# Optimization experiments

Hardware: AMD Instinct MI355X
Metric: run time of the kernel (lower is better)

The kernel has to match this reference:

```python
import jax, jax.numpy as jnp
import numpy as np

L, NK = 4, 6  # num blocks, Nk geodesic components

def _gelu(x):
    return jax.nn.gelu(x, approximate=False)  # torch nn.GELU default (erf)

def _ln(x, g, b, eps=1e-5):
    m = jnp.mean(x, axis=-1, keepdims=True)
    v = jnp.mean((x - m) ** 2, axis=-1, keepdims=True)
    return (x - m) * jax.lax.rsqrt(v + eps) * g + b


def setup_inputs() -> dict:
    B, N, C, M = 4, 8192, 64, 64
    key = jax.random.key(0)
    ks = iter(jax.random.split(key, 48))
    def nrm(*s):
        return jax.random.normal(next(ks), s, dtype=jnp.float32) * 0.02
    inp = {
        'x': jax.random.normal(next(ks), (B, N, 1), dtype=jnp.float32),
        'MATRIX_Phy': jax.random.normal(next(ks), (N, M), dtype=jnp.float32) * 0.02,
        'INVERSE_Phy': jax.random.normal(next(ks), (M, N), dtype=jnp.float32) * 0.02,
        'meshPoints': jax.random.normal(next(ks), (N, 3), dtype=jnp.float32),
        'adj_norm': jax.random.uniform(next(ks), (N, N), dtype=jnp.float32) / N,
    }
    inp.update(
        fc0_w=nrm(4, C), fc0_b=jnp.zeros(C), fc01_w=nrm(C, C), fc01_b=jnp.zeros(C),
        blk_ln1_g=jnp.ones((L, C)), blk_ln1_b=jnp.zeros((L, C)),
        norm1_g=jnp.ones((L, C)), norm1_b=jnp.zeros((L, C)),
        spec_w=jax.random.uniform(next(ks), (L, NK, C, C, M), dtype=jnp.float32) / (C * C),
        enc_p1_w=nrm(L, 3, C), enc_p1_b=jnp.zeros((L, C)),
        enc_p2_w=nrm(L, C, C), enc_p2_b=jnp.zeros((L, C)),
        enc_g1_w=nrm(L, C, C), enc_g1_b=jnp.zeros((L, C)),
        enc_g2_w=nrm(L, C, C), enc_g2_b=jnp.zeros((L, C)),
        enc_o1_w=nrm(L, C, 2 * C), enc_o1_b=jnp.zeros((L, 2 * C)),
        enc_o2_w=nrm(L, 2 * C, NK), enc_o2_b=jnp.zeros((L, NK)),
        spat_g1_w=nrm(L, C, 2 * C), spat_g1_b=jnp.zeros((L, 2 * C)),
        spat_g2_w=nrm(L, 2 * C, C), spat_g2_b=jnp.zeros((L, C)),
        blk_ln2_g=jnp.ones((L, C)), blk_ln2_b=jnp.zeros((L, C)),
        mlp_pre_w=nrm(L, C, 2 * C), mlp_pre_b=jnp.zeros((L, 2 * C)),
        mlp_post_w=nrm(L, 2 * C, C), mlp_post_b=jnp.zeros((L, C)),
        ln1_g=jnp.ones(C), ln1_b=jnp.zeros(C),
        fc1_w=nrm(C, 128), fc1_b=jnp.zeros(128),
        fc2_w=nrm(128, 1), fc2_b=jnp.zeros(1),
    )
    return inp


def reference(x, MATRIX_Phy, INVERSE_Phy, meshPoints, adj_norm,
              fc0_w, fc0_b, fc01_w, fc01_b,
              blk_ln1_g, blk_ln1_b, norm1_g, norm1_b, spec_w,
              enc_p1_w, enc_p1_b, enc_p2_w, enc_p2_b,
              enc_g1_w, enc_g1_b, enc_g2_w, enc_g2_b,
              enc_o1_w, enc_o1_b, enc_o2_w, enc_o2_b,
              spat_g1_w, spat_g1_b, spat_g2_w, spat_g2_b,
              blk_ln2_g, blk_ln2_b, mlp_pre_w, mlp_pre_b, mlp_post_w, mlp_post_b,
              ln1_g, ln1_b, fc1_w, fc1_b, fc2_w, fc2_b):
    B = x.shape[0]
    mesh = jnp.broadcast_to(meshPoints[None], (B,) + meshPoints.shape)  # [B,N,3]
    h = jnp.concatenate([x, mesh], axis=-1)                             # [B,N,4]
    h = h @ fc0_w + fc0_b
    h = h @ fc01_w + fc01_b                                             # [B,N,C]
    for l in range(L):
        z = _ln(h, blk_ln1_g[l], blk_ln1_b[l])
        # --- MeshGCN encoder -> geodesic mixing coefficients geoT [M,Nk] ---
        e = _gelu(meshPoints @ enc_p1_w[l] + enc_p1_b[l]) @ enc_p2_w[l] + enc_p2_b[l]
        e = _gelu(adj_norm @ (e @ enc_g1_w[l] + enc_g1_b[l]))
        e = adj_norm @ (e @ enc_g2_w[l] + enc_g2_b[l])
        e = (e @ enc_o1_w[l] + enc_o1_b[l]) @ enc_o2_w[l] + enc_o2_b[l]  # [N,Nk]
        geoT = jax.nn.softmax(INVERSE_Phy @ e, axis=1)                   # [M,Nk]
        # --- geodesic-modulated spectral conv ---
        cm = jnp.einsum('mn,bnc->bcm', INVERSE_Phy, z)                   # [B,C,M]
        w = jnp.einsum('kiom,mk->iom', spec_w[l], geoT)                  # [C,C,M]
        cg = jnp.einsum('bim,iom->bom', cm, w)                           # [B,C,M]
        x1 = jnp.einsum('bom,nm->bno', cg, MATRIX_Phy)                   # [B,N,C]
        x1 = _ln(x1, norm1_g[l], norm1_b[l])
        # --- spatial GCN branch (SimpleGCN: gcn->relu->gcn) ---
        s = jax.nn.relu(jnp.einsum('mn,bnc->bmc', adj_norm, z @ spat_g1_w[l] + spat_g1_b[l]))
        x2 = jnp.einsum('mn,bnc->bmc', adj_norm, s @ spat_g2_w[l] + spat_g2_b[l])
        h = x1 + x2 + h
        z2 = _ln(h, blk_ln2_g[l], blk_ln2_b[l])
        h = _gelu(z2 @ mlp_pre_w[l] + mlp_pre_b[l]) @ mlp_post_w[l] + mlp_post_b[l] + h
    h = _gelu(_ln(h, ln1_g, ln1_b) @ fc1_w + fc1_b)
    return h @ fc2_w + fc2_b                                             # [B,N,1]
```

## Files before the change

kernel.cpp:

```cpp
#include <hip/hip_runtime.h>
#include <math.h>

typedef __bf16 bf16_t;
typedef __bf16 bf16x8 __attribute__((ext_vector_type(8)));
typedef __bf16 bf16x4 __attribute__((ext_vector_type(4)));
typedef float  f32x4  __attribute__((ext_vector_type(4)));
typedef float  f32x16 __attribute__((ext_vector_type(16)));

#define NN 8192
#define RA 8320
#define GPS256 2129920u
#define XPAD 68
#define X2PAD 132
#define ZTPAD 66

__device__ __forceinline__ float gelu_f(float x) {
    return 0.5f * x * (1.0f + erff(x * 0.70710678118654752f));
}

__device__ __forceinline__ float wsum64(float v) {
#pragma unroll
    for (int m = 32; m; m >>= 1) v += __shfl_xor(v, m);
    return v;
}

__device__ __forceinline__ float gpn(const float* __restrict__ Gp, size_t gi, size_t st, int ns) {
    float v = Gp[gi];
    if (ns == 2) v += Gp[gi + st];
    return v;
}

__device__ __forceinline__ void async16(const void* g, void* l) {
    __builtin_amdgcn_global_load_lds(
        (const __attribute__((address_space(1))) unsigned int*)g,
        (__attribute__((address_space(3))) unsigned int*)l,
        16, 0, 0);
}

__device__ __forceinline__ void mm16(const float* __restrict__ X, int xpad,
                                     const float* __restrict__ W, int ws, int K,
                                     int c, int r0, float* acc) {
    for (int k0 = 0; k0 < K; k0 += 4) {
        float w0 = W[(size_t)(k0 + 0) * ws + c];
        float w1 = W[(size_t)(k0 + 1) * ws + c];
        float w2 = W[(size_t)(k0 + 2) * ws + c];
        float w3 = W[(size_t)(k0 + 3) * ws + c];
#pragma unroll
        for (int i = 0; i < 16; ++i) {
            float4 xv = *(const float4*)(X + (size_t)(r0 + i) * xpad + k0);
            acc[i] = fmaf(xv.x, w0, acc[i]);
            acc[i] = fmaf(xv.y, w1, acc[i]);
            acc[i] = fmaf(xv.z, w2, acc[i]);
            acc[i] = fmaf(xv.w, w3, acc[i]);
        }
    }
}

__global__ __launch_bounds__(256) void k_adj_convert(const float* __restrict__ adj,
                                                     const float* __restrict__ INV,
                                                     bf16_t* __restrict__ adjB,
                                                     float* __restrict__ rowsum) {
    int row = blockIdx.x;
    int t = threadIdx.x;
    bf16_t* br = adjB + (size_t)row * NN;
    if (row >= NN + 64) {
        bf16x4 zz; zz[0] = zz[1] = zz[2] = zz[3] = (bf16_t)0.f;
#pragma unroll
        for (int v = 0; v < 8; ++v) *(bf16x4*)(br + (v * 256 + t) * 4) = zz;
        return;
    }
    const float* ar = (row < NN) ? adj + (size_t)row * NN : INV + (size_t)(row - NN) * NN;
    float s = 0.f;
#pragma unroll
    for (int v = 0; v < 8; ++v) {
        int i = (v * 256 + t) * 4;
        float4 f = *(const float4*)(ar + i);
        s += f.x + f.y + f.z + f.w;
        bf16x4 o;
        o[0] = (bf16_t)f.x; o[1] = (bf16_t)f.y; o[2] = (bf16_t)f.z; o[3] = (bf16_t)f.w;
        *(bf16x4*)(br + i) = o;
    }
    if (row < NN) {
        s = wsum64(s);
        __shared__ float w4[4];
        if ((t & 63) == 0) w4[t >> 6] = s;
        __syncthreads();
        if (t == 0) rowsum[row] = w4[0] + w4[1] + w4[2] + w4[3];
    }
}

__global__ __launch_bounds__(64) void k_fold(const float* __restrict__ fc0w, const float* __restrict__ fc0b,
                                             const float* __restrict__ fc01w, const float* __restrict__ fc01b,
                                             float* __restrict__ W0b) {
    int c = threadIdx.x;
#pragma unroll
    for (int j = 0; j < 4; ++j) {
        float a = 0.f;
        for (int k = 0; k < 64; ++k) a += fc0w[j * 64 + k] * fc01w[k * 64 + c];
        W0b[j * 64 + c] = a;
    }
    float b = fc01b[c];
    for (int k = 0; k < 64; ++k) b += fc0b[k] * fc01w[k * 64 + c];
    W0b[256 + c] = b;
}

__global__ __launch_bounds__(256) void k_init_h(const float* __restrict__ x, const float* __restrict__ mesh,
                         const float* __restrict__ W0b,
                         const float* __restrict__ zg, const float* __restrict__ zb,
                         float* __restrict__ h, bf16_t* __restrict__ Vt) {
    __shared__ __align__(16) char buf[64 * ZTPAD * 2];
    bf16_t* ZT = (bf16_t*)buf;
    int t = threadIdx.x, c = t & 63, rq = t >> 6, r0 = rq * 16;
    int bb = blockIdx.x >> 7, n0 = (blockIdx.x & 127) * 64;
    float w0c = W0b[c], w1c = W0b[64 + c], w2c = W0b[128 + c], w3c = W0b[192 + c], b0c = W0b[256 + c];
    float gc = zg[c], bc = zb[c];
#pragma unroll
    for (int q = 0; q < 16; ++q) {
        int n = n0 + r0 + q;
        int w = bb * NN + n;
        float xv = x[w];
        float m0 = mesh[n * 3], m1 = mesh[n * 3 + 1], m2 = mesh[n * 3 + 2];
        float hv = b0c + xv * w0c + m0 * w1c + m1 * w2c + m2 * w3c;
        h[(size_t)w * 64 + c] = hv;
        float s = wsum64(hv), s2 = wsum64(hv * hv);
        float mean = s * (1.f / 64.f), var = s2 * (1.f / 64.f) - mean * mean;
        float z = (hv - mean) * rsqrtf(var + 1e-5f) * gc + bc;
        ZT[c * ZTPAD + r0 + q] = (bf16_t)z;
    }
    __syncthreads();
#pragma unroll
    for (int cc = 0; cc < 16; ++cc) {
        int c2 = r0 + cc;
        Vt[(size_t)(256 + bb * 64 + c2) * NN + n0 + c] = ZT[c2 * ZTPAD + c];
    }
}

__global__ __launch_bounds__(256) void k_enc_pre(const float* __restrict__ mesh,
                          const float* __restrict__ p1w, const float* __restrict__ p1b,
                          const float* __restrict__ p2w, const float* __restrict__ p2b,
                          const float* __restrict__ g1w, const float* __restrict__ g1b,
                          bf16_t* __restrict__ Vt) {
    __shared__ __align__(16) char buf[2 * 64 * XPAD * 4];
    float* X1 = (float*)buf;
    float* X2 = (float*)(buf + 64 * XPAD * 4);
    bf16_t* ZT = (bf16_t*)buf;
    int t = threadIdx.x, c = t & 63, rq = t >> 6, r0 = rq * 16;
    int ll = blockIdx.x >> 7, n0 = (blockIdx.x & 127) * 64;
    float p1b_c = p1b[ll * 64 + c];
    float p1w0 = p1w[(ll * 3 + 0) * 64 + c], p1w1 = p1w[(ll * 3 + 1) * 64 + c], p1w2 = p1w[(ll * 3 + 2) * 64 + c];
#pragma unroll
    for (int q = 0; q < 16; ++q) {
        int n = n0 + r0 + q;
        float m0 = mesh[n * 3], m1 = mesh[n * 3 + 1], m2 = mesh[n * 3 + 2];
        X1[(r0 + q) * XPAD + c] = gelu_f(p1b_c + m0 * p1w0 + m1 * p1w1 + m2 * p1w2);
    }
    __syncthreads();
    float e2[16];
#pragma unroll
    for (int i = 0; i < 16; ++i) e2[i] = p2b[ll * 64 + c];
    mm16(X1, XPAD, p2w + ll * 4096, 64, 64, c, r0, e2);
    __syncthreads();
#pragma unroll
    for (int q = 0; q < 16; ++q) X2[(r0 + q) * XPAD + c] = e2[q];
    __syncthreads();
    float tt[16];
#pragma unroll
    for (int i = 0; i < 16; ++i) tt[i] = g1b[ll * 64 + c];
    mm16(X2, XPAD, g1w + ll * 4096, 64, 64, c, r0, tt);
#pragma unroll
    for (int q = 0; q < 16; ++q) ZT[c * ZTPAD + r0 + q] = (bf16_t)tt[q];
    __syncthreads();
#pragma unroll
    for (int cc = 0; cc < 16; ++cc) {
        int c2 = r0 + cc;
        Vt[(size_t)(ll * 64 + c2) * NN + n0 + c] = ZT[c2 * ZTPAD + c];
    }
}

__global__ __launch_bounds__(256) void k_enc_mid(const float* __restrict__ Gp,
                          const float* __restrict__ g2w, const float* __restrict__ g2b,
                          bf16_t* __restrict__ Vt) {
    __shared__ __align__(16) char buf[64 * XPAD * 4 + 64 * ZTPAD * 2];
    float* X = (float*)buf;
    bf16_t* ZT = (bf16_t*)(buf + 64 * XPAD * 4);
    int t = threadIdx.x, c = t & 63, rq = t >> 6, r0 = rq * 16;
    int ll = blockIdx.x >> 7, n0 = (blockIdx.x & 127) * 64;
#pragma unroll
    for (int q = 0; q < 16; ++q) {
        int n = n0 + r0 + q;
        size_t gi = (size_t)n * 256 + ll * 64 + c;
        X[(r0 + q) * XPAD + c] = gelu_f(Gp[gi] + Gp[gi + GPS256]);
    }
    __syncthreads();
    float t2[16];
#pragma unroll
    for (int i = 0; i < 16; ++i) t2[i] = g2b[ll * 64 + c];
    mm16(X, XPAD, g2w + ll * 4096, 64, 64, c, r0, t2);
#pragma unroll
    for (int q = 0; q < 16; ++q) ZT[c * ZTPAD + r0 + q] = (bf16_t)t2[q];
    __syncthreads();
#pragma unroll
    for (int cc = 0; cc < 16; ++cc) {
        int c2 = r0 + cc;
        Vt[(size_t)(ll * 64 + c2) * NN + n0 + c] = ZT[c2 * ZTPAD + c];
    }
}

__global__ void k_geo_part(const float* __restrict__ Gp,
                           const float* __restrict__ o1w, const float* __restrict__ o1b,
                           const float* __restrict__ o2w, const float* __restrict__ o2b,
                           const float* __restrict__ INV,
                           float* __restrict__ partials) {
    int l = blockIdx.x >> 7, chunk = blockIdx.x & 127;
    int n0 = chunk * 64;
    int t = threadIdx.x;
    __shared__ float e4L[64][65];
    for (int r = 0; r < 64; ++r)
        e4L[r][t] = Gp[(size_t)(n0 + r) * 512 + l * 64 + t];
    __syncthreads();
    float X[64];
#pragma unroll
    for (int i = 0; i < 64; ++i) X[i] = e4L[t][i];
    float e5[6] = {0, 0, 0, 0, 0, 0};
    const float* o1wl = o1w + (size_t)l * 64 * 128;
    const float* o2wl = o2w + (size_t)l * 128 * 6;
    for (int j = 0; j < 128; ++j) {
        float a = o1b[l * 128 + j];
#pragma unroll
        for (int i = 0; i < 64; ++i) a += X[i] * o1wl[i * 128 + j];
#pragma unroll
        for (int k = 0; k < 6; ++k) e5[k] += a * o2wl[j * 6 + k];
    }
#pragma unroll
    for (int k = 0; k < 6; ++k) e5[k] += o2b[l * 6 + k];
    __shared__ float e5L[64][8];
#pragma unroll
    for (int k = 0; k < 6; ++k) e5L[t][k] = e5[k];
    __syncthreads();
    float p[6] = {0, 0, 0, 0, 0, 0};
    const float* ivr = INV + (size_t)t * NN + n0;
    for (int r = 0; r < 64; ++r) {
        float iv = ivr[r];
#pragma unroll
        for (int k = 0; k < 6; ++k) p[k] += iv * e5L[r][k];
    }
#pragma unroll
    for (int k = 0; k < 6; ++k) partials[(size_t)(((l * 128 + chunk) * 64) + t) * 6 + k] = p[k];
}

__global__ void k_geo_final(const float* __restrict__ partials, float* __restrict__ geoT) {
    int l = blockIdx.x, m = threadIdx.x;
    float g[6] = {0, 0, 0, 0, 0, 0};
    for (int ch = 0; ch < 128; ++ch) {
#pragma unroll
        for (int k = 0; k < 6; ++k) g[k] += partials[(size_t)(((l * 128 + ch) * 64) + m) * 6 + k];
    }
    float mx = g[0];
#pragma unroll
    for (int k = 1; k < 6; ++k) mx = fmaxf(mx, g[k]);
    float s = 0.f;
#pragma unroll
    for (int k = 0; k < 6; ++k) { g[k] = expf(g[k] - mx); s += g[k]; }
    float inv = 1.f / s;
#pragma unroll
    for (int k = 0; k < 6; ++k) geoT[(size_t)(l * 64 + m) * 6 + k] = g[k] * inv;
}

__global__ __launch_bounds__(64) void k_w(const float* __restrict__ specw,
                                          const float* __restrict__ geoT,
                                          float* __restrict__ wAll) {
    int l = blockIdx.x >> 12, io = blockIdx.x & 4095;
    int m = threadIdx.x;
    float a = 0.f;
#pragma unroll
    for (int k = 0; k < 6; ++k)
        a += specw[(((size_t)l * 6 + k) * 4096 + io) * 64 + m] * geoT[(size_t)(l * 64 + m) * 6 + k];
    wAll[((size_t)l * 4096 + io) * 64 + m] = a;
}

__global__ __launch_bounds__(256) void k_cmsum(const float* __restrict__ Gp, float* __restrict__ cmc,
                                               int ncols, int colbase, int ns) {
    int bi = blockIdx.x * 4 + (threadIdx.x >> 6);
    int m = threadIdx.x & 63;
    size_t st = (size_t)RA * ncols;
    size_t gi = (size_t)(NN + m) * ncols + colbase + bi;
    cmc[bi * 64 + m] = gpn(Gp, gi, st, ns);
}

__global__ __launch_bounds__(256) void k_cg2(const float* __restrict__ cmc,
                                             const float* __restrict__ wl,
                                             float* __restrict__ cgT) {
    int o = blockIdx.x;
    int b = threadIdx.x >> 6, m = threadIdx.x & 63;
    float acc = 0.f;
    for (int i = 0; i < 64; ++i)
        acc += cmc[(b * 64 + i) * 64 + m] * wl[((size_t)(i * 64 + o)) * 64 + m];
    cgT[(b * 64 + m) * 64 + o] = acc;
}

__global__ __launch_bounds__(256) void k_spat_mid(const float* __restrict__ Gp,
                           const float* __restrict__ W1, const float* __restrict__ b1,
                           const float* __restrict__ W2, const float* __restrict__ b2,
                           const float* __restrict__ rowsum, bf16_t* __restrict__ Vt,
                           int ncols, int colbase, int ns) {
    __shared__ __align__(16) char buf[64 * XPAD * 4 + 64 * X2PAD * 4];
    float* X  = (float*)buf;
    float* X2 = (float*)(buf + 64 * XPAD * 4);
    bf16_t* ZT = (bf16_t*)buf;
    int t = threadIdx.x, c = t & 63, rq = t >> 6, r0 = rq * 16;
    int bb = blockIdx.x >> 7, n0 = (blockIdx.x & 127) * 64;
    size_t st = (size_t)RA * ncols;
    float rs[16];
#pragma unroll
    for (int q = 0; q < 16; ++q) {
        int m = n0 + r0 + q;
        rs[q] = rowsum[m];
        X[(r0 + q) * XPAD + c] = gpn(Gp, (size_t)m * ncols + colbase + bb * 64 + c, st, ns);
    }
    __syncthreads();
    float ma0[16], ma1[16];
    float b1c0 = b1[c], b1c1 = b1[64 + c];
#pragma unroll
    for (int i = 0; i < 16; ++i) { ma0[i] = rs[i] * b1c0; ma1[i] = rs[i] * b1c1; }
    mm16(X, XPAD, W1, 128, 64, c, r0, ma0);
    mm16(X, XPAD, W1 + 64, 128, 64, c, r0, ma1);
    __syncthreads();
#pragma unroll
    for (int q = 0; q < 16; ++q) {
        X2[(r0 + q) * X2PAD + c] = fmaxf(ma0[q], 0.f);
        X2[(r0 + q) * X2PAD + 64 + c] = fmaxf(ma1[q], 0.f);
    }
    __syncthreads();
    float y[16];
#pragma unroll
    for (int i = 0; i < 16; ++i) y[i] = b2[c];
    mm16(X2, X2PAD, W2, 64, 128, c, r0, y);
#pragma unroll
    for (int q = 0; q < 16; ++q) ZT[c * ZTPAD + r0 + q] = (bf16_t)y[q];
    __syncthreads();
#pragma unroll
    for (int cc = 0; cc < 16; ++cc) {
        int c2 = r0 + cc;
        Vt[(size_t)(bb * 64 + c2) * NN + n0 + c] = ZT[c2 * ZTPAD + c];
    }
}

__global__ __launch_bounds__(256) void k_blk_post(float* __restrict__ h, const float* __restrict__ Gp,
                           const float* __restrict__ cgT, const float* __restrict__ MP,
                           const float* __restrict__ n1g, const float* __restrict__ n1b,
                           const float* __restrict__ l2g, const float* __restrict__ l2b,
                           const float* __restrict__ prew, const float* __restrict__ preb,
                           const float* __restrict__ postw, const float* __restrict__ postb,
                           const float* __restrict__ zng, const float* __restrict__ znb,
                           bf16_t* __restrict__ Vt, int writeZ) {
    __shared__ __align__(16) char buf[64 * X2PAD * 4 + 64 * XPAD * 4];
    float* MProws = (float*)buf;
    float* X2     = (float*)buf;
    float* X      = (float*)(buf + 64 * X2PAD * 4);
    bf16_t* ZT    = (bf16_t*)(buf + 64 * X2PAD * 4);
    int t = threadIdx.x, c = t & 63, rq = t >> 6, r0 = rq * 16;
    int bb = blockIdx.x >> 7, n0 = (blockIdx.x & 127) * 64;
#pragma unroll
    for (int q = 0; q < 16; ++q)
        MProws[(r0 + q) * XPAD + c] = MP[(size_t)(n0 + r0 + q) * 64 + c];
    __syncthreads();
    float x1[16];
#pragma unroll
    for (int i = 0; i < 16; ++i) x1[i] = 0.f;
    mm16(MProws, XPAD, cgT + (size_t)bb * 4096, 64, 64, c, r0, x1);
    float hv[16];
    float n1gc = n1g[c], n1bc = n1b[c];
#pragma unroll
    for (int q = 0; q < 16; ++q) {
        float s = wsum64(x1[q]), s2 = wsum64(x1[q] * x1[q]);
        float mean = s * (1.f / 64.f), var = s2 * (1.f / 64.f) - mean * mean;
        float x1n = (x1[q] - mean) * rsqrtf(var + 1e-5f) * n1gc + n1bc;
        int n = n0 + r0 + q;
        size_t w = (size_t)bb * NN + n;
        size_t gi = (size_t)n * 256 + bb * 64 + c;
        hv[q] = x1n + (Gp[gi] + Gp[gi + GPS256]) + h[w * 64 + c];
    }
    float l2gc = l2g[c], l2bc = l2b[c];
#pragma unroll
    for (int q = 0; q < 16; ++q) {
        float s = wsum64(hv[q]), s2 = wsum64(hv[q] * hv[q]);
        float mean = s * (1.f / 64.f), var = s2 * (1.f / 64.f) - mean * mean;
        X[(r0 + q) * XPAD + c] = (hv[q] - mean) * rsqrtf(var + 1e-5f) * l2gc + l2bc;
    }
    __syncthreads();
    float ma0[16], ma1[16];
    float pb0 = preb[c], pb1 = preb[64 + c];
#pragma unroll
    for (int i = 0; i < 16; ++i) { ma0[i] = pb0; ma1[i] = pb1; }
    mm16(X, XPAD, prew, 128, 64, c, r0, ma0);
    mm16(X, XPAD, prew + 64, 128, 64, c, r0, ma1);
    __syncthreads();
#pragma unroll
    for (int q = 0; q < 16; ++q) {
        X2[(r0 + q) * X2PAD + c] = gelu_f(ma0[q]);
        X2[(r0 + q) * X2PAD + 64 + c] = gelu_f(ma1[q]);
    }
    __syncthreads();
    float o[16];
    float pob = postb[c];
#pragma unroll
    for (int i = 0; i < 16; ++i) o[i] = pob;
    mm16(X2, X2PAD, postw, 64, 128, c, r0, o);
#pragma unroll
    for (int q = 0; q < 16; ++q) {
        hv[q] += o[q];
        h[((size_t)bb * NN + n0 + r0 + q) * 64 + c] = hv[q];
    }
    if (writeZ) {
        float zgc = zng[c], zbc = znb[c];
#pragma unroll
        for (int q = 0; q < 16; ++q) {
            float s = wsum64(hv[q]), s2 = wsum64(hv[q] * hv[q]);
            float mean = s * (1.f / 64.f), var = s2 * (1.f / 64.f) - mean * mean;
            ZT[c * ZTPAD + r0 + q] = (bf16_t)((hv[q] - mean) * rsqrtf(var + 1e-5f) * zgc + zbc);
        }
        __syncthreads();
#pragma unroll
        for (int cc = 0; cc < 16; ++cc) {
            int c2 = r0 + cc;
            Vt[(size_t)(256 + bb * 64 + c2) * NN + n0 + c] = ZT[c2 * ZTPAD + c];
        }
    }
}

__global__ __launch_bounds__(256) void k_head(const float* __restrict__ h,
                       const float* __restrict__ g, const float* __restrict__ bb_,
                       const float* __restrict__ fc1w, const float* __restrict__ fc1b,
                       const float* __restrict__ fc2w, const float* __restrict__ fc2b,
                       float* __restrict__ out) {
    __shared__ __align__(16) char buf[64 * XPAD * 4 + 64 * X2PAD * 4];
    float* X  = (float*)buf;
    float* X2 = (float*)(buf + 64 * XPAD * 4);
    int t = threadIdx.x, c = t & 63, rq = t >> 6, r0 = rq * 16;
    int bb = blockIdx.x >> 7, n0 = (blockIdx.x & 127) * 64;
    float gc = g[c], bc = bb_[c];
#pragma unroll
    for (int q = 0; q < 16; ++q) {
        float hv = h[((size_t)bb * NN + n0 + r0 + q) * 64 + c];
        float s = wsum64(hv), s2 = wsum64(hv * hv);
        float mean = s * (1.f / 64.f), var = s2 * (1.f / 64.f) - mean * mean;
        X[(r0 + q) * XPAD + c] = (hv - mean) * rsqrtf(var + 1e-5f) * gc + bc;
    }
    __syncthreads();
    float ma0[16], ma1[16];
    float fb0 = fc1b[c], fb1 = fc1b[64 + c];
#pragma unroll
    for (int i = 0; i < 16; ++i) { ma0[i] = fb0; ma1[i] = fb1; }
    mm16(X, XPAD, fc1w, 128, 64, c, r0, ma0);
    mm16(X, XPAD, fc1w + 64, 128, 64, c, r0, ma1);
    __syncthreads();
#pragma unroll
    for (int q = 0; q < 16; ++q) {
        X2[(r0 + q) * X2PAD + c] = gelu_f(ma0[q]);
        X2[(r0 + q) * X2PAD + 64 + c] = gelu_f(ma1[q]);
    }
    __syncthreads();
    float f2a = fc2w[c], f2b = fc2w[64 + c], f2bias = fc2b[0];
#pragma unroll
    for (int q = 0; q < 16; ++q) {
        float val = X2[(r0 + q) * X2PAD + c] * f2a + X2[(r0 + q) * X2PAD + 64 + c] * f2b;
        val = wsum64(val);
        if (c == 0) out[(size_t)bb * NN + n0 + r0 + q] = val + f2bias;
    }
}

__global__ __launch_bounds__(256) void gemm_bf16(const bf16_t* __restrict__ A,
                                                 const bf16_t* __restrict__ Bt,
                                                 float* __restrict__ Gp,
                                                 int ntn, int ns) {
    __shared__ __align__(16) char smem[2][24576];
    const int cpx = gridDim.x >> 3;
    const int bid = blockIdx.x;
    const int tile = (bid & 7) * cpx + (bid >> 3);
    const int pertile = 65 * ntn;
    const int ks = tile / pertile;
    const int r2 = tile % pertile;
    const int tn = r2 & (ntn - 1);
    const int tm = r2 / ntn;
    const int nkt = 128 / ns;
    const int kt0 = ks * nkt;
    const int ncols = ntn * 64;

    const int t = threadIdx.x;
    const int lane = t & 63, wid = t >> 6;
    const int wr = wid >> 1, wc = wid & 1;
    const int lm = lane & 31;
    const int lkg = lane >> 5;

    const bf16_t* Abase = A + (size_t)tm * 128 * NN;
    const bf16_t* Bbase = Bt + (size_t)tn * 64 * NN;

    f32x16 acc0, acc1;
#pragma unroll
    for (int i = 0; i < 16; ++i) { acc0[i] = 0.f; acc1[i] = 0.f; }

    auto stage = [&](int bsel, int kt) {
        char* lb = smem[bsel];
        int k0 = kt * 64;
#pragma unroll
        for (int r = 0; r < 4; ++r) {
            int ci = t + r * 256;
            int rw = ci >> 3, ch = ci & 7;
            int sch = ch ^ (rw & 7);
            async16(Abase + (size_t)rw * NN + k0 + sch * 8, lb + ci * 16);
        }
#pragma unroll
        for (int r = 0; r < 2; ++r) {
            int ci = t + r * 256;
            int rw = ci >> 3, ch = ci & 7;
            int sch = ch ^ (rw & 7);
            async16(Bbase + (size_t)rw * NN + k0 + sch * 8, lb + 16384 + ci * 16);
        }
    };

    const int R0 = wr * 64 + lm;
    const int R1 = R0 + 32;
    const int Q  = wc * 32 + lm;
    const int swzA = R0 & 7, swzB = Q & 7;

    stage(0, kt0);
    __syncthreads();
    for (int it = 0; it < nkt; ++it) {
        int cur = it & 1;
        if (it + 1 < nkt) stage(cur ^ 1, kt0 + it + 1);
        const char* lb = smem[cur];
#pragma unroll
        for (int ks4 = 0; ks4 < 4; ++ks4) {
            int kc = ks4 * 2 + lkg;
            bf16x8 av0 = *(const bf16x8*)(lb + R0 * 128 + ((kc ^ swzA) << 4));
            bf16x8 av1 = *(const bf16x8*)(lb + R1 * 128 + ((kc ^ swzA) << 4));
            bf16x8 bv  = *(const bf16x8*)(lb + 16384 + Q * 128 + ((kc ^ swzB) << 4));
            acc0 = __builtin_amdgcn_mfma_f32_32x32x16_bf16(av0, bv, acc0, 0, 0, 0);
            acc1 = __builtin_amdgcn_mfma_f32_32x32x16_bf16(av1, bv, acc1, 0, 0, 0);
        }
        __syncthreads();
    }

    float* Cs = Gp + (size_t)ks * RA * ncols;
    const int colg = tn * 64 + wc * 32 + lm;
    const int rbase0 = tm * 128 + wr * 64 + 4 * lkg;
#pragma unroll
    for (int reg = 0; reg < 16; ++reg) {
        int rrow = (reg & 3) + 8 * (reg >> 2);
        Cs[(size_t)(rbase0 + rrow) * ncols + colg] = acc0[reg];
    }
#pragma unroll
    for (int reg = 0; reg < 16; ++reg) {
        int rrow = (reg & 3) + 8 * (reg >> 2);
        Cs[(size_t)(rbase0 + 32 + rrow) * ncols + colg] = acc1[reg];
    }
}


extern "C" void kernel_launch(void* const* d_in, const int* in_sizes, int n_in,
                              void* d_out, int out_size, void* d_ws, size_t ws_size,
                              hipStream_t stream) {
    const float* x     = (const float*)d_in[0];
    const float* MP    = (const float*)d_in[1];
    const float* INV   = (const float*)d_in[2];
    const float* mesh  = (const float*)d_in[3];
    const float* adj   = (const float*)d_in[4];
    const float* fc0w  = (const float*)d_in[5];
    const float* fc0b  = (const float*)d_in[6];
    const float* fc01w = (const float*)d_in[7];
    const float* fc01b = (const float*)d_in[8];
    const float* bln1g = (const float*)d_in[9];
    const float* bln1b = (const float*)d_in[10];
    const float* n1g   = (const float*)d_in[11];
    const float* n1b   = (const float*)d_in[12];
    const float* specw = (const float*)d_in[13];
    const float* p1w   = (const float*)d_in[14];
    const float* p1b   = (const float*)d_in[15];
    const float* p2w   = (const float*)d_in[16];
    const float* p2b   = (const float*)d_in[17];
    const float* g1w   = (const float*)d_in[18];
    const float* g1b   = (const float*)d_in[19];
    const float* g2w   = (const float*)d_in[20];
    const float* g2b   = (const float*)d_in[21];
    const float* o1w   = (const float*)d_in[22];
    const float* o1b   = (const float*)d_in[23];
    const float* o2w   = (const float*)d_in[24];
    const float* o2b   = (const float*)d_in[25];
    const float* sg1w  = (const float*)d_in[26];
    const float* sg1b  = (const float*)d_in[27];
    const float* sg2w  = (const float*)d_in[28];
    const float* sg2b  = (const float*)d_in[29];
    const float* bln2g = (const float*)d_in[30];
    const float* bln2b = (const float*)d_in[31];
    const float* prew  = (const float*)d_in[32];
    const float* preb  = (const float*)d_in[33];
    const float* postw = (const float*)d_in[34];
    const float* postb = (const float*)d_in[35];
    const float* ln1g  = (const float*)d_in[36];
    const float* ln1b  = (const float*)d_in[37];
    const float* fc1w  = (const float*)d_in[38];
    const float* fc1b  = (const float*)d_in[39];
    const float* fc2w  = (const float*)d_in[40];
    const float* fc2b  = (const float*)d_in[41];
    float* out = (float*)d_out;

    char* ws = (char*)d_ws;
    bf16_t* adjB    = (bf16_t*)(ws);
    float*  Gp512   = (float*) (ws + 136314880);
    float*  Gp256   = (float*) (ws + 153354240);
    bf16_t* Vt      = (bf16_t*)(ws + 170393600);
    float*  h       = (float*) (ws + 178782208);
    float*  rowsum  = (float*) (ws + 187170816);
    float*  partials= (float*) (ws + 187203584);
    float*  geoT    = (float*) (ws + 187990016);
    float*  wAll    = (float*) (ws + 187996160);
    float*  cmc     = (float*) (ws + 192190464);
    float*  cgT     = (float*) (ws + 192256000);
    float*  W0b     = (float*) (ws + 192321536);

    bf16_t* VtZ = Vt + (size_t)256 * NN;

    k_adj_convert<<<RA, 256, 0, stream>>>(adj, INV, adjB, rowsum);
    k_fold<<<1, 64, 0, stream>>>(fc0w, fc0b, fc01w, fc01b, W0b);

    k_enc_pre<<<512, 256, 0, stream>>>(mesh, p1w, p1b, p2w, p2b, g1w, g1b, Vt);
    gemm_bf16<<<520, 256, 0, stream>>>(adjB, Vt, Gp256, 4, 2);
    k_enc_mid<<<512, 256, 0, stream>>>(Gp256, g2w, g2b, Vt);
    k_init_h<<<512, 256, 0, stream>>>(x, mesh, W0b, bln1g, bln1b, h, Vt);

    gemm_bf16<<<520, 256, 0, stream>>>(adjB, Vt, Gp512, 8, 1);

    k_geo_part<<<512, 64, 0, stream>>>(Gp512, o1w, o1b, o2w, o2b, INV, partials);
    k_geo_final<<<4, 64, 0, stream>>>(partials, geoT);
    k_w<<<16384, 64, 0, stream>>>(specw, geoT, wAll);

    for (int l = 0; l < 4; ++l) {
        const float* Gp1 = Gp256; int nc = 256, cb = 0, ns1 = 2;
        if (l == 0) { Gp1 = Gp512; nc = 512; cb = 256; ns1 = 1; }
        else {
            gemm_bf16<<<520, 256, 0, stream>>>(adjB, VtZ, Gp256, 4, 2);
        }
        k_cmsum<<<64, 256, 0, stream>>>(Gp1, cmc, nc, cb, ns1);
        k_cg2<<<64, 256, 0, stream>>>(cmc, wAll + (size_t)l * 262144, cgT);
        k_spat_mid<<<512, 256, 0, stream>>>(Gp1, sg1w + l * 64 * 128, sg1b + l * 128,
                                            sg2w + l * 128 * 64, sg2b + l * 64, rowsum, Vt,
                                            nc, cb, ns1);
        gemm_bf16<<<520, 256, 0, stream>>>(adjB, Vt, Gp256, 4, 2);
        int ln = (l < 3) ? (l + 1) : 3;
        k_blk_post<<<512, 256, 0, stream>>>(h, Gp256, cgT, MP,
                                            n1g + l * 64, n1b + l * 64,
                                            bln2g + l * 64, bln2b + l * 64,
                                            prew + l * 64 * 128, preb + l * 128,
                                            postw + l * 128 * 64, postb + l * 64,
                                            bln1g + ln * 64, bln1b + ln * 64,
                                            Vt, (l < 3) ? 1 : 0);
    }

    k_head<<<512, 256, 0, stream>>>(h, ln1g, ln1b, fc1w, fc1b, fc2w, fc2b, out);
}
```

Baseline: 1.377 ms.

## Widen adjacency GEMM tile to 128x256 with 512 threads and more split-K

The bf16 adjacency GEMM now uses 512-thread blocks, each computing a 128x256 output tile with a 2x2 set of MFMA accumulators per wave, so each A tile loaded from the large adjacency matrix is reused across more columns. To keep enough blocks in flight, split-K goes from 2 to 4 (and 1 to 2 for the wide GEMM), and every consumer kernel now sums four (or two) partial slices. The workspace is enlarged to hold the extra partials, which adds reduction reads and partial-buffer traffic in exchange for fewer re-reads of the adjacency matrix. The launch-bounds hint of two blocks per CU with doubled shared memory may also limit occupancy.

```diff
diff --git a/kernel.cpp b/kernel.cpp
--- a/kernel.cpp
+++ b/kernel.cpp
@@ -10,6 +10,7 @@
 #define NN 8192
 #define RA 8320
 #define GPS256 2129920u
+#define GPS512 4259840u
 #define XPAD 68
 #define X2PAD 132
 #define ZTPAD 66
@@ -24,9 +25,13 @@
     return v;
 }
 
+__device__ __forceinline__ float gp4(const float* __restrict__ Gp, size_t gi) {
+    return (Gp[gi] + Gp[gi + (size_t)GPS256]) + (Gp[gi + 2 * (size_t)GPS256] + Gp[gi + 3 * (size_t)GPS256]);
+}
+
 __device__ __forceinline__ float gpn(const float* __restrict__ Gp, size_t gi, size_t st, int ns) {
     float v = Gp[gi];
-    if (ns == 2) v += Gp[gi + st];
+    for (int s = 1; s < ns; ++s) v += Gp[gi + (size_t)s * st];
     return v;
 }
 
@@ -188,8 +193,7 @@
 #pragma unroll
     for (int q = 0; q < 16; ++q) {
         int n = n0 + r0 + q;
-        size_t gi = (size_t)n * 256 + ll * 64 + c;
-        X[(r0 + q) * XPAD + c] = gelu_f(Gp[gi] + Gp[gi + GPS256]);
+        X[(r0 + q) * XPAD + c] = gelu_f(gp4(Gp, (size_t)n * 256 + ll * 64 + c));
     }
     __syncthreads();
     float t2[16];
@@ -215,8 +219,10 @@
     int n0 = chunk * 64;
     int t = threadIdx.x;
     __shared__ float e4L[64][65];
-    for (int r = 0; r < 64; ++r)
-        e4L[r][t] = Gp[(size_t)(n0 + r) * 512 + l * 64 + t];
+    for (int r = 0; r < 64; ++r) {
+        size_t gi = (size_t)(n0 + r) * 512 + l * 64 + t;
+        e4L[r][t] = Gp[gi] + Gp[gi + (size_t)GPS512];
+    }
     __syncthreads();
     float X[64];
 #pragma unroll
@@ -377,8 +383,7 @@
         float x1n = (x1[q] - mean) * rsqrtf(var + 1e-5f) * n1gc + n1bc;
         int n = n0 + r0 + q;
         size_t w = (size_t)bb * NN + n;
-        size_t gi = (size_t)n * 256 + bb * 64 + c;
-        hv[q] = x1n + (Gp[gi] + Gp[gi + GPS256]) + h[w * 64 + c];
+        hv[q] = x1n + gp4(Gp, (size_t)n * 256 + bb * 64 + c) + h[w * 64 + c];
     }
     float l2gc = l2g[c], l2bc = l2b[c];
 #pragma unroll
@@ -469,49 +474,51 @@
     }
 }
 
-__global__ __launch_bounds__(256) void gemm_bf16(const bf16_t* __restrict__ A,
-                                                 const bf16_t* __restrict__ Bt,
-                                                 float* __restrict__ Gp,
-                                                 int ntn, int ns) {
-    __shared__ __align__(16) char smem[2][24576];
-    const int cpx = gridDim.x >> 3;
+__global__ __launch_bounds__(512, 2) void gemm_bf16(const bf16_t* __restrict__ A,
+                                                    const bf16_t* __restrict__ Bt,
+                                                    float* __restrict__ Gp,
+                                                    int ntn, int ns) {
+    __shared__ __align__(16) char smem[2][49152];
     const int bid = blockIdx.x;
-    const int tile = (bid & 7) * cpx + (bid >> 3);
-    const int pertile = 65 * ntn;
-    const int ks = tile / pertile;
-    const int r2 = tile % pertile;
-    const int tn = r2 & (ntn - 1);
-    const int tm = r2 / ntn;
+    const int per_tm = ntn * ns;
+    const int tm = bid / per_tm;
+    const int rem = bid % per_tm;
+    const int tn = rem / ns;
+    const int ks = rem % ns;
     const int nkt = 128 / ns;
     const int kt0 = ks * nkt;
-    const int ncols = ntn * 64;
+    const int ncols = ntn * 256;
 
     const int t = threadIdx.x;
     const int lane = t & 63, wid = t >> 6;
-    const int wr = wid >> 1, wc = wid & 1;
+    const int wr = wid >> 2, wc = wid & 3;
     const int lm = lane & 31;
     const int lkg = lane >> 5;
 
     const bf16_t* Abase = A + (size_t)tm * 128 * NN;
-    const bf16_t* Bbase = Bt + (size_t)tn * 64 * NN;
-
-    f32x16 acc0, acc1;
-#pragma unroll
-    for (int i = 0; i < 16; ++i) { acc0[i] = 0.f; acc1[i] = 0.f; }
+    const bf16_t* Bbase = Bt + (size_t)tn * 256 * NN;
+
+    f32x16 acc[2][2];
+#pragma unroll
+    for (int i = 0; i < 2; ++i)
+#pragma unroll
+        for (int j = 0; j < 2; ++j)
+#pragma unroll
+            for (int r = 0; r < 16; ++r) acc[i][j][r] = 0.f;
 
     auto stage = [&](int bsel, int kt) {
         char* lb = smem[bsel];
         int k0 = kt * 64;
 #pragma unroll
-        for (int r = 0; r < 4; ++r) {
-            int ci = t + r * 256;
+        for (int r = 0; r < 2; ++r) {
+            int ci = t + r * 512;
             int rw = ci >> 3, ch = ci & 7;
             int sch = ch ^ (rw & 7);
             async16(Abase + (size_t)rw * NN + k0 + sch * 8, lb + ci * 16);
         }
 #pragma unroll
-        for (int r = 0; r < 2; ++r) {
-            int ci = t + r * 256;
+        for (int r = 0; r < 4; ++r) {
+            int ci = t + r * 512;
             int rw = ci >> 3, ch = ci & 7;
             int sch = ch ^ (rw & 7);
             async16(Bbase + (size_t)rw * NN + k0 + sch * 8, lb + 16384 + ci * 16);
@@ -520,8 +527,9 @@
 
     const int R0 = wr * 64 + lm;
     const int R1 = R0 + 32;
-    const int Q  = wc * 32 + lm;
-    const int swzA = R0 & 7, swzB = Q & 7;
+    const int Q0 = wc * 64 + lm;
+    const int Q1 = Q0 + 32;
+    const int swzA = R0 & 7, swzB = Q0 & 7;
 
     stage(0, kt0);
     __syncthreads();
@@ -534,26 +542,28 @@
             int kc = ks4 * 2 + lkg;
             bf16x8 av0 = *(const bf16x8*)(lb + R0 * 128 + ((kc ^ swzA) << 4));
             bf16x8 av1 = *(const bf16x8*)(lb + R1 * 128 + ((kc ^ swzA) << 4));
-            bf16x8 bv  = *(const bf16x8*)(lb + 16384 + Q * 128 + ((kc ^ swzB) << 4));
-            acc0 = __builtin_amdgcn_mfma_f32_32x32x16_bf16(av0, bv, acc0, 0, 0, 0);
-            acc1 = __builtin_amdgcn_mfma_f32_32x32x16_bf16(av1, bv, acc1, 0, 0, 0);
+            bf16x8 bv0 = *(const bf16x8*)(lb + 16384 + Q0 * 128 + ((kc ^ swzB) << 4));
+            bf16x8 bv1 = *(const bf16x8*)(lb + 16384 + Q1 * 128 + ((kc ^ swzB) << 4));
+            acc[0][0] = __builtin_amdgcn_mfma_f32_32x32x16_bf16(av0, bv0, acc[0][0], 0, 0, 0);
+            acc[0][1] = __builtin_amdgcn_mfma_f32_32x32x16_bf16(av0, bv1, acc[0][1], 0, 0, 0);
+            acc[1][0] = __builtin_amdgcn_mfma_f32_32x32x16_bf16(av1, bv0, acc[1][0], 0, 0, 0);
+            acc[1][1] = __builtin_amdgcn_mfma_f32_32x32x16_bf16(av1, bv1, acc[1][1], 0, 0, 0);
         }
         __syncthreads();
     }
 
     float* Cs = Gp + (size_t)ks * RA * ncols;
-    const int colg = tn * 64 + wc * 32 + lm;
-    const int rbase0 = tm * 128 + wr * 64 + 4 * lkg;
-#pragma unroll
-    for (int reg = 0; reg < 16; ++reg) {
-        int rrow = (reg & 3) + 8 * (reg >> 2);
-        Cs[(size_t)(rbase0 + rrow) * ncols + colg] = acc0[reg];
-    }
-#pragma unroll
-    for (int reg = 0; reg < 16; ++reg) {
-        int rrow = (reg & 3) + 8 * (reg >> 2);
-        Cs[(size_t)(rbase0 + 32 + rrow) * ncols + colg] = acc1[reg];
-    }
+    const int colbase = tn * 256 + wc * 64 + lm;
+    const int rowbase = tm * 128 + wr * 64 + 4 * lkg;
+#pragma unroll
+    for (int i = 0; i < 2; ++i)
+#pragma unroll
+        for (int j = 0; j < 2; ++j)
+#pragma unroll
+            for (int reg = 0; reg < 16; ++reg) {
+                int rrow = (reg & 3) + 8 * (reg >> 2);
+                Cs[(size_t)(rowbase + i * 32 + rrow) * ncols + colbase + j * 32] = acc[i][j][reg];
+            }
 }
 
 
@@ -607,16 +617,16 @@
     char* ws = (char*)d_ws;
     bf16_t* adjB    = (bf16_t*)(ws);
     float*  Gp512   = (float*) (ws + 136314880);
-    float*  Gp256   = (float*) (ws + 153354240);
-    bf16_t* Vt      = (bf16_t*)(ws + 170393600);
-    float*  h       = (float*) (ws + 178782208);
-    float*  rowsum  = (float*) (ws + 187170816);
-    float*  partials= (float*) (ws + 187203584);
-    float*  geoT    = (float*) (ws + 187990016);
-    float*  wAll    = (float*) (ws + 187996160);
-    float*  cmc     = (float*) (ws + 192190464);
-    float*  cgT     = (float*) (ws + 192256000);
-    float*  W0b     = (float*) (ws + 192321536);
+    float*  Gp256   = (float*) (ws + 170393600);
+    bf16_t* Vt      = (bf16_t*)(ws + 204472320);
+    float*  h       = (float*) (ws + 212860928);
+    float*  rowsum  = (float*) (ws + 221249536);
+    float*  partials= (float*) (ws + 221282304);
+    float*  geoT    = (float*) (ws + 222068736);
+    float*  wAll    = (float*) (ws + 222074880);
+    float*  cmc     = (float*) (ws + 226269184);
+    float*  cgT     = (float*) (ws + 226334720);
+    float*  W0b     = (float*) (ws + 226400256);
 
     bf16_t* VtZ = Vt + (size_t)256 * NN;
 
@@ -624,28 +634,28 @@
     k_fold<<<1, 64, 0, stream>>>(fc0w, fc0b, fc01w, fc01b, W0b);
 
     k_enc_pre<<<512, 256, 0, stream>>>(mesh, p1w, p1b, p2w, p2b, g1w, g1b, Vt);
-    gemm_bf16<<<520, 256, 0, stream>>>(adjB, Vt, Gp256, 4, 2);
+    gemm_bf16<<<260, 512, 0, stream>>>(adjB, Vt, Gp256, 1, 4);
     k_enc_mid<<<512, 256, 0, stream>>>(Gp256, g2w, g2b, Vt);
     k_init_h<<<512, 256, 0, stream>>>(x, mesh, W0b, bln1g, bln1b, h, Vt);
 
-    gemm_bf16<<<520, 256, 0, stream>>>(adjB, Vt, Gp512, 8, 1);
+    gemm_bf16<<<260, 512, 0, stream>>>(adjB, Vt, Gp512, 2, 2);
 
     k_geo_part<<<512, 64, 0, stream>>>(Gp512, o1w, o1b, o2w, o2b, INV, partials);
     k_geo_final<<<4, 64, 0, stream>>>(partials, geoT);
     k_w<<<16384, 64, 0, stream>>>(specw, geoT, wAll);
 
     for (int l = 0; l < 4; ++l) {
-        const float* Gp1 = Gp256; int nc = 256, cb = 0, ns1 = 2;
-        if (l == 0) { Gp1 = Gp512; nc = 512; cb = 256; ns1 = 1; }
+        const float* Gp1 = Gp256; int nc = 256, cb = 0, ns1 = 4;
+        if (l == 0) { Gp1 = Gp512; nc = 512; cb = 256; ns1 = 2; }
         else {
-            gemm_bf16<<<520, 256, 0, stream>>>(adjB, VtZ, Gp256, 4, 2);
+            gemm_bf16<<<260, 512, 0, stream>>>(adjB, VtZ, Gp256, 1, 4);
         }
         k_cmsum<<<64, 256, 0, stream>>>(Gp1, cmc, nc, cb, ns1);
         k_cg2<<<64, 256, 0, stream>>>(cmc, wAll + (size_t)l * 262144, cgT);
         k_spat_mid<<<512, 256, 0, stream>>>(Gp1, sg1w + l * 64 * 128, sg1b + l * 128,
                                             sg2w + l * 128 * 64, sg2b + l * 64, rowsum, Vt,
                                             nc, cb, ns1);
-        gemm_bf16<<<520, 256, 0, stream>>>(adjB, Vt, Gp256, 4, 2);
+        gemm_bf16<<<260, 512, 0, stream>>>(adjB, Vt, Gp256, 1, 4);
         int ln = (l < 3) ? (l + 1) : 3;
         k_blk_post<<<512, 256, 0, stream>>>(h, Gp256, cgT, MP,
                                             n1g + l * 64, n1b + l * 64,
```

Result: slower. 1.514 ms (+9.9%).
